# Performance work log

Hardware: AMD Instinct MI355X
Metric: run time of the kernel (lower is better)

Reference implementation:

```python
import jax, jax.numpy as jnp
import numpy as np

N_NODES = 100000
N_EDGES = 1600000
IN_FEATS = 64
NUM_CLASSES = 64


def setup_inputs() -> dict:
    key = jax.random.key(0)
    k1, k2, k3, k4, k5, k6 = jax.random.split(key, 6)
    in_feat = jax.random.normal(k1, (N_NODES, IN_FEATS), dtype=jnp.float32)
    src = jax.random.randint(k2, (N_EDGES,), 0, N_NODES, dtype=jnp.int32)
    dst = jax.random.randint(k3, (N_EDGES,), 0, N_NODES, dtype=jnp.int32)
    scale = 1.0 / np.sqrt(IN_FEATS)
    W_self = jax.random.normal(k4, (IN_FEATS, NUM_CLASSES), dtype=jnp.float32) * scale
    W_neigh = jax.random.normal(k5, (IN_FEATS, NUM_CLASSES), dtype=jnp.float32) * scale
    bias = jax.random.normal(k6, (NUM_CLASSES,), dtype=jnp.float32) * 0.01
    return {"in_feat": in_feat, "src": src, "dst": dst,
            "W_self": W_self, "W_neigh": W_neigh, "bias": bias}


def reference(in_feat, src, dst, W_self, W_neigh, bias):
    # SAGEConv with 'mean' aggregator (DGL semantics):
    #   h_neigh[v] = mean over incoming edges (u->v) of in_feat[u]; 0 if no in-edges
    #   out = fc_self(x) + fc_neigh(h_neigh) + bias, then sigmoid
    n = in_feat.shape[0]
    msg = in_feat[src]                                            # [E, F] gather
    agg = jax.ops.segment_sum(msg, dst, num_segments=n)           # [N, F]
    deg = jax.ops.segment_sum(jnp.ones((src.shape[0],), jnp.float32), dst,
                              num_segments=n)                     # [N]
    h_neigh = agg / jnp.maximum(deg, 1.0)[:, None]                # mean, 0 for isolated
    out = in_feat @ W_self + h_neigh @ W_neigh + bias
    return jax.nn.sigmoid(out)
```

## Files before the change

kernel.cpp:

```cpp
#include <hip/hip_runtime.h>


constexpr int NN = 100000;
constexpr int NE = 1600000;
constexpr int F  = 64;
constexpr int RB = 256;
constexpr int NB = (NN + RB - 1) / RB;
constexpr int CH = 8192;
constexpr int PB = (NE + CH - 1) / CH;
constexpr int PREPB = (NN * F / 8 + 1024 + 255) / 256;
constexpr int QSZ = 25000;
constexpr int NP  = 9;
constexpr int SCAP = 2048;

typedef short bf16x8 __attribute__((ext_vector_type(8)));
typedef float f32x4  __attribute__((ext_vector_type(4)));
typedef float f32x2  __attribute__((ext_vector_type(2)));
typedef unsigned short u16;
typedef u16 u16x8 __attribute__((ext_vector_type(8)));
typedef unsigned u32x4 __attribute__((ext_vector_type(4)));

__device__ __forceinline__ u16 f2bf(float f) {
    unsigned u = __float_as_uint(f);
    unsigned r = (u + 0x7FFF + ((u >> 16) & 1)) >> 16;
    return (u16)r;
}

__device__ __forceinline__ void acc8pk(f32x2& a0, f32x2& a1, f32x2& a2, f32x2& a3,
                                       int2 qq) {
#if __has_builtin(__builtin_amdgcn_cvt_pk_f32_fp8)
    a0 += __builtin_amdgcn_cvt_pk_f32_fp8(qq.x, false);
    a1 += __builtin_amdgcn_cvt_pk_f32_fp8(qq.x, true);
    a2 += __builtin_amdgcn_cvt_pk_f32_fp8(qq.y, false);
    a3 += __builtin_amdgcn_cvt_pk_f32_fp8(qq.y, true);
#else
    a0[0] += __builtin_amdgcn_cvt_f32_fp8(qq.x, 0);
    a0[1] += __builtin_amdgcn_cvt_f32_fp8(qq.x, 1);
    a1[0] += __builtin_amdgcn_cvt_f32_fp8(qq.x, 2);
    a1[1] += __builtin_amdgcn_cvt_f32_fp8(qq.x, 3);
    a2[0] += __builtin_amdgcn_cvt_f32_fp8(qq.y, 0);
    a2[1] += __builtin_amdgcn_cvt_f32_fp8(qq.y, 1);
    a3[0] += __builtin_amdgcn_cvt_f32_fp8(qq.y, 2);
    a3[1] += __builtin_amdgcn_cvt_f32_fp8(qq.y, 3);
#endif
}

__global__ __launch_bounds__(256) void k_prep_hist(
    const float* __restrict__ x, const float* __restrict__ Ws,
    const float* __restrict__ Wn, const int* __restrict__ dst,
    unsigned char* __restrict__ x8, u16* __restrict__ xb, u16* __restrict__ Bt,
    int* __restrict__ gcount, int* __restrict__ donecnt,
    int* __restrict__ basep, int* __restrict__ cursor)
{
    const int bid = blockIdx.x;
    const int t   = threadIdx.x;

    if (bid < PREPB) {
        const int i = bid * 256 + t;
        if (i < NN * F / 8) {
            const int o = i * 8;
            float4 a = *(const float4*)&x[o];
            float4 b = *(const float4*)&x[o + 4];
            int lo = 0, hi = 0;
            lo = __builtin_amdgcn_cvt_pk_fp8_f32(a.x, a.y, lo, false);
            lo = __builtin_amdgcn_cvt_pk_fp8_f32(a.z, a.w, lo, true);
            hi = __builtin_amdgcn_cvt_pk_fp8_f32(b.x, b.y, hi, false);
            hi = __builtin_amdgcn_cvt_pk_fp8_f32(b.z, b.w, hi, true);
            *(int2*)&x8[o] = make_int2(lo, hi);
            u16x8 r;
            r[0] = f2bf(a.x); r[1] = f2bf(a.y); r[2] = f2bf(a.z); r[3] = f2bf(a.w);
            r[4] = f2bf(b.x); r[5] = f2bf(b.y); r[6] = f2bf(b.z); r[7] = f2bf(b.w);
            __builtin_nontemporal_store(*(u32x4*)&r, (u32x4*)&xb[o]);
        } else if (i < NN * F / 8 + 1024) {
            const int j  = i - NN * F / 8;
            const int n  = j >> 4;
            const int kb = (j & 15) * 8;
            u16x8 r;
#pragma unroll
            for (int jj = 0; jj < 8; ++jj) {
                const int kk = kb + jj;
                const float w = (kk < 64) ? Ws[kk * 64 + n] : Wn[(kk - 64) * 64 + n];
                r[jj] = f2bf(w);
            }
            *(u16x8*)&Bt[n * 128 + kb] = r;
        }
        return;
    }

    __shared__ int h[NB];
    __shared__ int lastflag;
    for (int i = t; i < NB; i += 256) h[i] = 0;
    __syncthreads();
    const int hb  = bid - PREPB;
    const int b0  = hb * CH;
    const int end = min(b0 + CH, NE);
    for (int i = b0 + t * 4; i < end; i += 1024) {
        int4 d = *(const int4*)&dst[i];
        atomicAdd(&h[d.x >> 8], 1);
        atomicAdd(&h[d.y >> 8], 1);
        atomicAdd(&h[d.z >> 8], 1);
        atomicAdd(&h[d.w >> 8], 1);
    }
    __syncthreads();
    for (int i = t; i < NB; i += 256)
        if (h[i]) atomicAdd(&gcount[i], h[i]);

    __threadfence();
    if (t == 0) lastflag = (atomicAdd(donecnt, 1) == PB - 1);
    __syncthreads();
    if (!lastflag || t >= 64) return;

    int v[7], pre[7], s = 0;
#pragma unroll
    for (int j = 0; j < 7; ++j) {
        const int idx = t * 7 + j;
        v[j] = (idx < NB) ? atomicAdd(&gcount[idx], 0) : 0;
        pre[j] = s;
        s += v[j];
    }
    int run = s;
#pragma unroll
    for (int o = 1; o < 64; o <<= 1) {
        const int n = __shfl_up(run, o);
        if (t >= o) run += n;
    }
    const int lbase = run - s;
#pragma unroll
    for (int j = 0; j < 7; ++j) {
        const int idx = t * 7 + j;
        if (idx < NB) {
            basep[idx]  = lbase + pre[j];
            cursor[idx] = lbase + pre[j];
        }
    }
}

__global__ __launch_bounds__(512) void k_part(const int* __restrict__ src,
                                              const int* __restrict__ dst,
                                              int* __restrict__ cursor,
                                              unsigned* __restrict__ packed) {
    __shared__ unsigned stage[CH];
    __shared__ unsigned short bkt[CH];
    __shared__ int hist[NB], lscan[NB], lcur[NB], gpos[NB];
    __shared__ int tmp[512];

    const int t   = threadIdx.x;
    const int b0  = blockIdx.x * CH;
    const int cnt = min(CH, NE - b0);

    for (int i = t; i < NB; i += 512) hist[i] = 0;
    __syncthreads();

    int4 sv[4], dv[4];
#pragma unroll
    for (int j = 0; j < 4; ++j) {
        const int idx = j * 2048 + t * 4;
        if (idx < cnt) {
            sv[j] = *(const int4*)&src[b0 + idx];
            dv[j] = *(const int4*)&dst[b0 + idx];
            atomicAdd(&hist[dv[j].x >> 8], 1);
            atomicAdd(&hist[dv[j].y >> 8], 1);
            atomicAdd(&hist[dv[j].z >> 8], 1);
            atomicAdd(&hist[dv[j].w >> 8], 1);
        }
    }
    __syncthreads();

    int val = (t < NB) ? hist[t] : 0;
    tmp[t] = val;
    __syncthreads();
    int s = val;
    for (int o = 1; o < 512; o <<= 1) {
        int add = (t >= o) ? tmp[t - o] : 0;
        __syncthreads();
        s += add;
        tmp[t] = s;
        __syncthreads();
    }
    if (t < NB) {
        lscan[t] = s - val;
        lcur[t]  = s - val;
        gpos[t]  = val ? atomicAdd(&cursor[t], val) : 0;
    }
    __syncthreads();

#pragma unroll
    for (int j = 0; j < 4; ++j) {
        const int idx = j * 2048 + t * 4;
        if (idx < cnt) {
            const int ss[4] = {sv[j].x, sv[j].y, sv[j].z, sv[j].w};
            const int dd[4] = {dv[j].x, dv[j].y, dv[j].z, dv[j].w};
#pragma unroll
            for (int q = 0; q < 4; ++q) {
                const int b   = dd[q] >> 8;
                const int qtr = ss[q] / QSZ;
                const int p   = atomicAdd(&lcur[b], 1);
                stage[p] = ((unsigned)(dd[q] & 255) << 19) |
                           ((unsigned)qtr << 17) | (unsigned)ss[q];
                bkt[p]   = (unsigned short)b;
            }
        }
    }
    __syncthreads();

    for (int i = t; i < cnt; i += 512) {
        const int b = bkt[i];
        __builtin_nontemporal_store(stage[i], &packed[gpos[b] + (i - lscan[b])]);
    }
}

__global__ __launch_bounds__(512) void k_fused(
    const unsigned char* __restrict__ x8, const u16* __restrict__ xb,
    const unsigned* __restrict__ packed, const int* __restrict__ basep,
    const u16* __restrict__ Bt, const float* __restrict__ bias,
    float* __restrict__ out)
{
    __shared__ u16 At[64 * 128];
    __shared__ unsigned stage[SCAP];
    __shared__ int hist[256], cur[256], exar[256];

    const int blk  = blockIdx.x;
    const int bu   = blk >> 2;
    const int qq   = blk & 3;
    const int base = bu * RB + qq * 64;
    const int t    = threadIdx.x;
    const int nv   = min(64, NN - base);

    const int e0 = basep[bu];
    const int e1 = (bu == NB - 1) ? NE : basep[bu + 1];
    const int m  = e1 - e0;

    if (t < 256) hist[t] = 0;
    __syncthreads();

    unsigned pv[NP];
#pragma unroll
    for (int j = 0; j < NP; ++j) {
        const int i = t + j * 512;
        unsigned p = 0xFFFFFFFFu;
        if (i < m) p = __builtin_nontemporal_load(&packed[e0 + i]);
        pv[j] = p;
        if (p != 0xFFFFFFFFu && (int)((p >> 25) & 3) == qq)
            atomicAdd(&hist[(p >> 17) & 255], 1);
    }
    for (int i = NP * 512 + t; i < m; i += 512) {
        const unsigned p = __builtin_nontemporal_load(&packed[e0 + i]);
        if ((int)((p >> 25) & 3) == qq) atomicAdd(&hist[(p >> 17) & 255], 1);
    }
    __syncthreads();

    if (t < 64) {
        const int v0 = hist[4 * t + 0], v1 = hist[4 * t + 1];
        const int v2 = hist[4 * t + 2], v3 = hist[4 * t + 3];
        const int sv = v0 + v1 + v2 + v3;
        int run = sv;
#pragma unroll
        for (int o = 1; o < 64; o <<= 1) {
            const int n = __shfl_up(run, o);
            if (t >= o) run += n;
        }
        const int b0 = run - sv;
        exar[4 * t + 0] = b0;
        exar[4 * t + 1] = b0 + v0;
        exar[4 * t + 2] = b0 + v0 + v1;
        exar[4 * t + 3] = b0 + v0 + v1 + v2;
        cur[4 * t + 0] = exar[4 * t + 0];
        cur[4 * t + 1] = exar[4 * t + 1];
        cur[4 * t + 2] = exar[4 * t + 2];
        cur[4 * t + 3] = exar[4 * t + 3];
    }
    __syncthreads();

#pragma unroll
    for (int j = 0; j < NP; ++j) {
        const unsigned p = pv[j];
        if (p != 0xFFFFFFFFu && (int)((p >> 25) & 3) == qq) {
            const int pos = atomicAdd(&cur[(p >> 17) & 255], 1);
            if (pos < SCAP) stage[pos] = p & 0x1FFFFu;
        }
    }
    for (int i = NP * 512 + t; i < m; i += 512) {
        const unsigned p = __builtin_nontemporal_load(&packed[e0 + i]);
        if ((int)((p >> 25) & 3) == qq) {
            const int pos = atomicAdd(&cur[(p >> 17) & 255], 1);
            if (pos < SCAP) stage[pos] = p & 0x1FFFFu;
        }
    }
    __syncthreads();

    const int r  = t >> 3;
    const int cg = t & 7;
    if (r < nv) {
        const int dg = hist[4 * r] + hist[4 * r + 1] + hist[4 * r + 2] + hist[4 * r + 3];
        const int s0 = exar[4 * r];
        f32x2 a0 = {0.f, 0.f}, a1 = a0, a2 = a0, a3 = a0;
        int e = 0;
        for (; e + 4 <= dg; e += 4) {
            const int i0 = stage[s0 + e + 0];
            const int i1 = stage[s0 + e + 1];
            const int i2 = stage[s0 + e + 2];
            const int i3 = stage[s0 + e + 3];
            int2 q0 = *(const int2*)&x8[(size_t)i0 * F + cg * 8];
            int2 q1 = *(const int2*)&x8[(size_t)i1 * F + cg * 8];
            int2 q2 = *(const int2*)&x8[(size_t)i2 * F + cg * 8];
            int2 q3 = *(const int2*)&x8[(size_t)i3 * F + cg * 8];
            acc8pk(a0, a1, a2, a3, q0);
            acc8pk(a0, a1, a2, a3, q1);
            acc8pk(a0, a1, a2, a3, q2);
            acc8pk(a0, a1, a2, a3, q3);
        }
        for (; e < dg; ++e) {
            int2 qv = *(const int2*)&x8[(size_t)stage[s0 + e] * F + cg * 8];
            acc8pk(a0, a1, a2, a3, qv);
        }
        const float inv = 1.0f / fmaxf((float)dg, 1.0f);
        u16x8 hbv;
        hbv[0] = f2bf(a0[0] * inv); hbv[1] = f2bf(a0[1] * inv);
        hbv[2] = f2bf(a1[0] * inv); hbv[3] = f2bf(a1[1] * inv);
        hbv[4] = f2bf(a2[0] * inv); hbv[5] = f2bf(a2[1] * inv);
        hbv[6] = f2bf(a3[0] * inv); hbv[7] = f2bf(a3[1] * inv);
        const int bh = (8 + cg) ^ (r & 15);
        *(u16x8*)&At[r * 128 + bh * 8] = hbv;

        u32x4 xw = __builtin_nontemporal_load((const u32x4*)&xb[(size_t)(base + r) * F + cg * 8]);
        const int bx = cg ^ (r & 15);
        *(u32x4*)&At[r * 128 + bx * 8] = xw;
    }
    __syncthreads();

    const int w    = t >> 6;
    const int lane = t & 63;
    const int tr   = w >> 1;
    if (tr * 16 >= nv) return;
    const int nh  = w & 1;
    const int r16 = lane & 15;
    const int kg  = lane >> 4;

    bf16x8 bfr[4][2];
#pragma unroll
    for (int t4 = 0; t4 < 4; ++t4)
#pragma unroll
        for (int uu = 0; uu < 2; ++uu) {
            const int n = (nh * 2 + uu) * 16 + r16;
            bfr[t4][uu] = *(const bf16x8*)&Bt[n * 128 + t4 * 32 + kg * 8];
        }
    const float b0 = bias[(nh * 2 + 0) * 16 + r16];
    const float b1 = bias[(nh * 2 + 1) * 16 + r16];

    const int row = tr * 16 + r16;
    bf16x8 a[4];
#pragma unroll
    for (int t4 = 0; t4 < 4; ++t4) {
        const int blk16 = (t4 * 4 + kg) ^ (row & 15);
        a[t4] = *(const bf16x8*)&At[row * 128 + blk16 * 8];
    }

    f32x4 c0 = {0.f, 0.f, 0.f, 0.f}, c1 = c0;
    c0 = __builtin_amdgcn_mfma_f32_16x16x32_bf16(a[0], bfr[0][0], c0, 0, 0, 0);
    c0 = __builtin_amdgcn_mfma_f32_16x16x32_bf16(a[1], bfr[1][0], c0, 0, 0, 0);
    c0 = __builtin_amdgcn_mfma_f32_16x16x32_bf16(a[2], bfr[2][0], c0, 0, 0, 0);
    c0 = __builtin_amdgcn_mfma_f32_16x16x32_bf16(a[3], bfr[3][0], c0, 0, 0, 0);
    c1 = __builtin_amdgcn_mfma_f32_16x16x32_bf16(a[0], bfr[0][1], c1, 0, 0, 0);
    c1 = __builtin_amdgcn_mfma_f32_16x16x32_bf16(a[1], bfr[1][1], c1, 0, 0, 0);
    c1 = __builtin_amdgcn_mfma_f32_16x16x32_bf16(a[2], bfr[2][1], c1, 0, 0, 0);
    c1 = __builtin_amdgcn_mfma_f32_16x16x32_bf16(a[3], bfr[3][1], c1, 0, 0, 0);

    float* orow = out + (size_t)(base + tr * 16) * 64;
#pragma unroll
    for (int rr = 0; rr < 4; ++rr) {
        const int ro = (kg * 4 + rr) * 64;
        __builtin_nontemporal_store(1.0f / (1.0f + __expf(-(c0[rr] + b0))),
                                    &orow[ro + (nh * 2 + 0) * 16 + r16]);
        __builtin_nontemporal_store(1.0f / (1.0f + __expf(-(c1[rr] + b1))),
                                    &orow[ro + (nh * 2 + 1) * 16 + r16]);
    }
}

extern "C" void kernel_launch(void* const* d_in, const int* in_sizes, int n_in,
                              void* d_out, int out_size, void* d_ws, size_t ws_size,
                              hipStream_t stream) {
    const float* x    = (const float*)d_in[0];
    const int*   src  = (const int*)d_in[1];
    const int*   dst  = (const int*)d_in[2];
    const float* Ws   = (const float*)d_in[3];
    const float* Wn   = (const float*)d_in[4];
    const float* bias = (const float*)d_in[5];
    float* out = (float*)d_out;

    int* gcount  = (int*)d_ws;
    int* donecnt = gcount + NB;
    int* basep   = donecnt + 1;
    int* cursor  = basep + NB;
    unsigned* packed = (unsigned*)(cursor + NB);
    unsigned char* x8 = (unsigned char*)(packed + NE);
    u16* xb = (u16*)(x8 + (size_t)NN * F);
    u16* Bt = xb + (size_t)NN * F;

    (void)hipMemsetAsync(gcount, 0, (size_t)(NB + 1) * sizeof(int), stream);

    k_prep_hist<<<PREPB + PB, 256, 0, stream>>>(x, Ws, Wn, dst, x8, xb, Bt,
                                                gcount, donecnt, basep, cursor);
    k_part <<<PB, 512, 0, stream>>>(src, dst, cursor, packed);
    k_fused<<<NB * 4, 512, 0, stream>>>(x8, xb, packed, basep, Bt, bias, out);
}
```

Baseline: 94.81 us.

## Add bucket-sort kernel producing CSR sources instead of per-block rescan

Adds a separate kernel that counting-sorts each 256-node bucket's packed edges by destination, writing a CSR offset array and sorted source indices. The fused kernel then reads its 64-node slice contiguously, with no histogram or scan, instead of four blocks each rescanning the whole bucket and filtering by source quarter. This removes the fourfold redundant read and atomics on packed edges but adds an extra launch plus a global write and read of the sorted sources. Nodes whose edges overflow the shared stage fall back to reading sources from global memory.

```diff
diff --git a/kernel.cpp b/kernel.cpp
--- a/kernel.cpp
+++ b/kernel.cpp
@@ -9,9 +9,8 @@
 constexpr int CH = 8192;
 constexpr int PB = (NE + CH - 1) / CH;
 constexpr int PREPB = (NN * F / 8 + 1024 + 255) / 256;
-constexpr int QSZ = 25000;
-constexpr int NP  = 9;
-constexpr int SCAP = 2048;
+constexpr int SCAP = 3072;
+constexpr int FB = (NN + 63) / 64;
 
 typedef short bf16x8 __attribute__((ext_vector_type(8)));
 typedef float f32x4  __attribute__((ext_vector_type(4)));
@@ -192,11 +191,9 @@
             const int dd[4] = {dv[j].x, dv[j].y, dv[j].z, dv[j].w};
 #pragma unroll
             for (int q = 0; q < 4; ++q) {
-                const int b   = dd[q] >> 8;
-                const int qtr = ss[q] / QSZ;
-                const int p   = atomicAdd(&lcur[b], 1);
-                stage[p] = ((unsigned)(dd[q] & 255) << 19) |
-                           ((unsigned)qtr << 17) | (unsigned)ss[q];
+                const int b = dd[q] >> 8;
+                const int p = atomicAdd(&lcur[b], 1);
+                stage[p] = ((unsigned)(dd[q] & 255) << 17) | (unsigned)ss[q];
                 bkt[p]   = (unsigned short)b;
             }
         }
@@ -209,109 +206,107 @@
     }
 }
 
+__global__ __launch_bounds__(256) void k_bsort(const unsigned* __restrict__ packed,
+                                               const int* __restrict__ basep,
+                                               int* __restrict__ ssrc,
+                                               int* __restrict__ off) {
+    __shared__ int hist[RB];
+    __shared__ int cur[RB];
+    const int b = blockIdx.x;
+    const int t = threadIdx.x;
+    const int e0 = basep[b];
+    const int e1 = (b == NB - 1) ? NE : basep[b + 1];
+    const int m  = e1 - e0;
+
+    hist[t] = 0;
+    __syncthreads();
+    for (int i = t; i < m; i += 256)
+        atomicAdd(&hist[packed[e0 + i] >> 17], 1);
+    __syncthreads();
+
+    const int val = hist[t];
+    cur[t] = val;
+    __syncthreads();
+    int s = val;
+    for (int o = 1; o < 256; o <<= 1) {
+        int add = (t >= o) ? cur[t - o] : 0;
+        __syncthreads();
+        s += add;
+        cur[t] = s;
+        __syncthreads();
+    }
+    const int ex = s - val;
+    const int v = b * RB + t;
+    if (v < NN) off[v] = e0 + ex;
+    cur[t] = ex;
+    __syncthreads();
+
+    for (int i = t; i < m; i += 256) {
+        const unsigned p = packed[e0 + i];
+        const int pos = atomicAdd(&cur[p >> 17], 1);
+        ssrc[e0 + pos] = (int)(p & 0x1FFFFu);
+    }
+}
+
 __global__ __launch_bounds__(512) void k_fused(
     const unsigned char* __restrict__ x8, const u16* __restrict__ xb,
-    const unsigned* __restrict__ packed, const int* __restrict__ basep,
+    const int* __restrict__ ssrc, const int* __restrict__ off,
     const u16* __restrict__ Bt, const float* __restrict__ bias,
     float* __restrict__ out)
 {
     __shared__ u16 At[64 * 128];
-    __shared__ unsigned stage[SCAP];
-    __shared__ int hist[256], cur[256], exar[256];
-
-    const int blk  = blockIdx.x;
-    const int bu   = blk >> 2;
-    const int qq   = blk & 3;
-    const int base = bu * RB + qq * 64;
+    __shared__ int stage[SCAP];
+    __shared__ int lofs[65];
+
+    const int base = blockIdx.x * 64;
     const int t    = threadIdx.x;
     const int nv   = min(64, NN - base);
 
-    const int e0 = basep[bu];
-    const int e1 = (bu == NB - 1) ? NE : basep[bu + 1];
-    const int m  = e1 - e0;
-
-    if (t < 256) hist[t] = 0;
-    __syncthreads();
-
-    unsigned pv[NP];
-#pragma unroll
-    for (int j = 0; j < NP; ++j) {
-        const int i = t + j * 512;
-        unsigned p = 0xFFFFFFFFu;
-        if (i < m) p = __builtin_nontemporal_load(&packed[e0 + i]);
-        pv[j] = p;
-        if (p != 0xFFFFFFFFu && (int)((p >> 25) & 3) == qq)
-            atomicAdd(&hist[(p >> 17) & 255], 1);
-    }
-    for (int i = NP * 512 + t; i < m; i += 512) {
-        const unsigned p = __builtin_nontemporal_load(&packed[e0 + i]);
-        if ((int)((p >> 25) & 3) == qq) atomicAdd(&hist[(p >> 17) & 255], 1);
-    }
-    __syncthreads();
-
-    if (t < 64) {
-        const int v0 = hist[4 * t + 0], v1 = hist[4 * t + 1];
-        const int v2 = hist[4 * t + 2], v3 = hist[4 * t + 3];
-        const int sv = v0 + v1 + v2 + v3;
-        int run = sv;
-#pragma unroll
-        for (int o = 1; o < 64; o <<= 1) {
-            const int n = __shfl_up(run, o);
-            if (t >= o) run += n;
-        }
-        const int b0 = run - sv;
-        exar[4 * t + 0] = b0;
-        exar[4 * t + 1] = b0 + v0;
-        exar[4 * t + 2] = b0 + v0 + v1;
-        exar[4 * t + 3] = b0 + v0 + v1 + v2;
-        cur[4 * t + 0] = exar[4 * t + 0];
-        cur[4 * t + 1] = exar[4 * t + 1];
-        cur[4 * t + 2] = exar[4 * t + 2];
-        cur[4 * t + 3] = exar[4 * t + 3];
-    }
-    __syncthreads();
-
-#pragma unroll
-    for (int j = 0; j < NP; ++j) {
-        const unsigned p = pv[j];
-        if (p != 0xFFFFFFFFu && (int)((p >> 25) & 3) == qq) {
-            const int pos = atomicAdd(&cur[(p >> 17) & 255], 1);
-            if (pos < SCAP) stage[pos] = p & 0x1FFFFu;
-        }
-    }
-    for (int i = NP * 512 + t; i < m; i += 512) {
-        const unsigned p = __builtin_nontemporal_load(&packed[e0 + i]);
-        if ((int)((p >> 25) & 3) == qq) {
-            const int pos = atomicAdd(&cur[(p >> 17) & 255], 1);
-            if (pos < SCAP) stage[pos] = p & 0x1FFFFu;
-        }
-    }
+    if (t <= 64) {
+        const int idx = base + t;
+        lofs[t] = (idx < NN) ? off[idx] : NE;
+    }
+    __syncthreads();
+    const int s_begin = lofs[0];
+    const int cnt     = lofs[nv] - s_begin;
+
+    const int ccap = min(cnt, SCAP);
+    for (int i = t; i < ccap; i += 512)
+        stage[i] = ssrc[s_begin + i];
     __syncthreads();
 
     const int r  = t >> 3;
     const int cg = t & 7;
     if (r < nv) {
-        const int dg = hist[4 * r] + hist[4 * r + 1] + hist[4 * r + 2] + hist[4 * r + 3];
-        const int s0 = exar[4 * r];
+        const int s0 = lofs[r] - s_begin;
+        const int dg = lofs[r + 1] - lofs[r];
         f32x2 a0 = {0.f, 0.f}, a1 = a0, a2 = a0, a3 = a0;
-        int e = 0;
-        for (; e + 4 <= dg; e += 4) {
-            const int i0 = stage[s0 + e + 0];
-            const int i1 = stage[s0 + e + 1];
-            const int i2 = stage[s0 + e + 2];
-            const int i3 = stage[s0 + e + 3];
-            int2 q0 = *(const int2*)&x8[(size_t)i0 * F + cg * 8];
-            int2 q1 = *(const int2*)&x8[(size_t)i1 * F + cg * 8];
-            int2 q2 = *(const int2*)&x8[(size_t)i2 * F + cg * 8];
-            int2 q3 = *(const int2*)&x8[(size_t)i3 * F + cg * 8];
-            acc8pk(a0, a1, a2, a3, q0);
-            acc8pk(a0, a1, a2, a3, q1);
-            acc8pk(a0, a1, a2, a3, q2);
-            acc8pk(a0, a1, a2, a3, q3);
-        }
-        for (; e < dg; ++e) {
-            int2 qv = *(const int2*)&x8[(size_t)stage[s0 + e] * F + cg * 8];
-            acc8pk(a0, a1, a2, a3, qv);
+        if (s0 + dg <= SCAP) {
+            int e = 0;
+            for (; e + 4 <= dg; e += 4) {
+                const int i0 = stage[s0 + e + 0];
+                const int i1 = stage[s0 + e + 1];
+                const int i2 = stage[s0 + e + 2];
+                const int i3 = stage[s0 + e + 3];
+                int2 q0 = *(const int2*)&x8[(size_t)i0 * F + cg * 8];
+                int2 q1 = *(const int2*)&x8[(size_t)i1 * F + cg * 8];
+                int2 q2 = *(const int2*)&x8[(size_t)i2 * F + cg * 8];
+                int2 q3 = *(const int2*)&x8[(size_t)i3 * F + cg * 8];
+                acc8pk(a0, a1, a2, a3, q0);
+                acc8pk(a0, a1, a2, a3, q1);
+                acc8pk(a0, a1, a2, a3, q2);
+                acc8pk(a0, a1, a2, a3, q3);
+            }
+            for (; e < dg; ++e) {
+                int2 qv = *(const int2*)&x8[(size_t)stage[s0 + e] * F + cg * 8];
+                acc8pk(a0, a1, a2, a3, qv);
+            }
+        } else {
+            for (int e = 0; e < dg; ++e) {
+                const int si = ssrc[lofs[r] + e];
+                int2 qv = *(const int2*)&x8[(size_t)si * F + cg * 8];
+                acc8pk(a0, a1, a2, a3, qv);
+            }
         }
         const float inv = 1.0f / fmaxf((float)dg, 1.0f);
         u16x8 hbv;
@@ -323,8 +318,7 @@
         *(u16x8*)&At[r * 128 + bh * 8] = hbv;
 
         u32x4 xw = __builtin_nontemporal_load((const u32x4*)&xb[(size_t)(base + r) * F + cg * 8]);
-        const int bx = cg ^ (r & 15);
-        *(u32x4*)&At[r * 128 + bx * 8] = xw;
+        *(u32x4*)&At[r * 128 + (cg ^ (r & 15)) * 8] = xw;
     }
     __syncthreads();
 
@@ -391,8 +385,10 @@
     int* donecnt = gcount + NB;
     int* basep   = donecnt + 1;
     int* cursor  = basep + NB;
-    unsigned* packed = (unsigned*)(cursor + NB);
-    unsigned char* x8 = (unsigned char*)(packed + NE);
+    int* off     = cursor + NB;
+    unsigned* packed = (unsigned*)(off + NN);
+    int* ssrc    = (int*)(packed + NE);
+    unsigned char* x8 = (unsigned char*)(ssrc + NE);
     u16* xb = (u16*)(x8 + (size_t)NN * F);
     u16* Bt = xb + (size_t)NN * F;
 
@@ -401,5 +397,6 @@
     k_prep_hist<<<PREPB + PB, 256, 0, stream>>>(x, Ws, Wn, dst, x8, xb, Bt,
                                                 gcount, donecnt, basep, cursor);
     k_part <<<PB, 512, 0, stream>>>(src, dst, cursor, packed);
-    k_fused<<<NB * 4, 512, 0, stream>>>(x8, xb, packed, basep, Bt, bias, out);
-}
+    k_bsort<<<NB, 256, 0, stream>>>(packed, basep, ssrc, off);
+    k_fused<<<FB, 512, 0, stream>>>(x8, xb, ssrc, off, Bt, bias, out);
+}
```

After: 103.7 us. 9.4% more time.
